# Optimization experiments

Measured on AMD Instinct MI355X. Metric: run time of the kernel, lower is better.

## Reference

```python
import jax, jax.numpy as jnp
import numpy as np

B, S, U, T = 64, 256, 1024, 512  # batch, max_sequence_size, units, output_token_length
W_SCALE = 0.02


def setup_inputs() -> dict:
    key = jax.random.key(0)
    ks = jax.random.split(key, 12)
    inp = {
        "h": jax.random.normal(ks[0], (B, S, U), jnp.float32),
        "s_0": jax.random.normal(ks[1], (B, U), jnp.float32),
        "Wy1": jax.random.normal(ks[2], (U, U), jnp.float32) * W_SCALE,
        "by1": jnp.zeros((U,), jnp.float32),
        "Wy2": jax.random.normal(ks[3], (U, T), jnp.float32) * W_SCALE,
        "by2": jnp.zeros((T,), jnp.float32),
        "We1": jax.random.normal(ks[4], (2 * U, U), jnp.float32) * W_SCALE,
        "be1": jnp.zeros((U,), jnp.float32),
        "We2": jax.random.normal(ks[5], (U, 1), jnp.float32) * W_SCALE,
        "be2": jnp.zeros((1,), jnp.float32),
        "Wf": jax.random.normal(ks[6], (T + U, U), jnp.float32) * W_SCALE,
        "bf": jnp.zeros((U,), jnp.float32),
        "Wi": jax.random.normal(ks[7], (T + U, U), jnp.float32) * W_SCALE,
        "bi": jnp.zeros((U,), jnp.float32),
        "Wg": jax.random.normal(ks[8], (T + U, U), jnp.float32) * W_SCALE,
        "bg": jnp.zeros((U,), jnp.float32),
        "Wo": jax.random.normal(ks[9], (T + U, U), jnp.float32) * W_SCALE,
        "bo": jnp.zeros((U,), jnp.float32),
    }
    return inp


def reference(h, s_0, Wy1, by1, Wy2, by2, We1, be1, We2, be2,
              Wf, bf, Wi, bi, Wg, bg, Wo, bo):
    # Precompute the h-dependent half of the first e_dense matmul once:
    # e_dense layer1 input is concat([h_i, s]) @ We1 = h_i @ We1[:U] + s @ We1[U:]
    We1_h, We1_s = We1[:U], We1[U:]
    h_proj = jnp.einsum('bsu,uv->bsv', h, We1_h)  # [B,S,U]

    def step(s, _):
        # y_dense: U -> U (tanh) -> T (linear)
        y = jnp.tanh(s @ Wy1 + by1) @ Wy2 + by2  # [B,T]
        # additive attention scores over all S encoder positions (vectorized)
        e1 = jax.nn.sigmoid(h_proj + (s @ We1_s + be1)[:, None, :])  # [B,S,U]
        e = jax.nn.sigmoid(jnp.squeeze(e1 @ We2, -1) + be2)          # [B,S]
        a = jax.nn.softmax(e, axis=-1)
        c = jnp.einsum('bsu,bs->bu', h, a)  # context vector [B,U]
        # LSTM cell with x = y, h = s, c = attention context
        x_h = jnp.concatenate([y, s], axis=-1)  # [B,T+U]
        i = jax.nn.sigmoid(x_h @ Wi + bi)
        f = jax.nn.sigmoid(x_h @ Wf + bf)
        o = jax.nn.sigmoid(x_h @ Wo + bo)
        g = jnp.tanh(x_h @ Wg + bg)
        c_new = f * c + i * g
        s_next = o * jnp.tanh(c_new)
        return s_next, y

    _, ys = jax.lax.scan(step, s_0, None, length=S)  # ys: [S,B,T]
    return jnp.transpose(ys, (1, 0, 2))  # [B,S,T]
```

## Files before the change

### kernel.cpp

```cpp
#include <hip/hip_runtime.h>
#include <hip/hip_bf16.h>

typedef __attribute__((ext_vector_type(4))) float floatx4;
typedef __attribute__((ext_vector_type(2))) float floatx2;
typedef __attribute__((ext_vector_type(8))) short shortx8;

#define NB 64
#define NS 256
#define NU 1024
#define NT 512

__device__ __forceinline__ unsigned short f2bf(float f){
  union{float f;unsigned u;}v; v.f=f;
  unsigned r = v.u + 0x7fffu + ((v.u>>16)&1u);
  return (unsigned short)(r>>16);
}
__device__ __forceinline__ float bf2f(unsigned short h){
  union{unsigned u;float f;}v; v.u = ((unsigned)h)<<16; return v.f;
}
__device__ __forceinline__ float sigf(float x){
  return __builtin_amdgcn_rcpf(1.f + __expf(-x));
}

__device__ __forceinline__ void cburst2x2f(floatx4 a[2], floatx4 b[2],
                                           const float* p0, const float* p1){
  asm volatile(
    "global_load_dwordx4 %0, %4, off sc0 sc1\n\t"
    "global_load_dwordx4 %1, %4, off offset:16 sc0 sc1\n\t"
    "global_load_dwordx4 %2, %5, off sc0 sc1\n\t"
    "global_load_dwordx4 %3, %5, off offset:16 sc0 sc1\n\t"
    "s_waitcnt vmcnt(0)"
    : "=&v"(a[0]),"=&v"(a[1]),"=&v"(b[0]),"=&v"(b[1])
    : "v"(p0),"v"(p1) : "memory");
}
__device__ __forceinline__ void cburst4d2(floatx2 o[4], const float* p0, const float* p1,
                                          const float* p2, const float* p3){
  asm volatile(
    "global_load_dwordx2 %0, %4, off sc0 sc1\n\t"
    "global_load_dwordx2 %1, %5, off sc0 sc1\n\t"
    "global_load_dwordx2 %2, %6, off sc0 sc1\n\t"
    "global_load_dwordx2 %3, %7, off sc0 sc1\n\t"
    "s_waitcnt vmcnt(0)"
    : "=&v"(o[0]),"=&v"(o[1]),"=&v"(o[2]),"=&v"(o[3])
    : "v"(p0),"v"(p1),"v"(p2),"v"(p3) : "memory");
}
__device__ __forceinline__ float cld_f32(const float* p){
  float v;
  asm volatile("global_load_dword %0, %1, off sc0 sc1\n\ts_waitcnt vmcnt(0)"
               : "=&v"(v) : "v"(p) : "memory");
  return v;
}
__device__ __forceinline__ void cst_u16(unsigned short* p, unsigned short v){
  asm volatile("global_store_short %0, %1, off sc0 sc1" :: "v"(p), "v"((unsigned)v) : "memory");
}
__device__ __forceinline__ void cst_f32(float* p, float v){
  asm volatile("global_store_dword %0, %1, off sc0 sc1" :: "v"(p), "v"(v) : "memory");
}
__device__ __forceinline__ void cst_u32(unsigned* p, unsigned v){
  asm volatile("global_store_dword %0, %1, off sc0 sc1" :: "v"(p), "v"(v) : "memory");
}

template<int MODE>
__global__ void gemm_sw(const unsigned short* __restrict__ A,
                        const unsigned short* __restrict__ Bsw,
                        void* __restrict__ Cout,
                        int M, int N, int K, int ldc,
                        const float* __restrict__ bias)
{
  const int lane = threadIdx.x & 63;
  const int lm = lane & 15, quad = lane >> 4;
  const int nwaves = (gridDim.x * blockDim.x) >> 6;
  const int w = (blockIdx.x * blockDim.x + threadIdx.x) >> 6;
  const int m64 = M >> 6, n64 = N >> 6, KS = K >> 5;
  const int ntask = m64 * n64;
  for (int task = w; task < ntask; task += nwaves) {
    const int mt = task % m64, nt = task / m64;
    floatx4 acc[4][4];
#pragma unroll
    for (int i=0;i<4;i++)
#pragma unroll
      for(int j=0;j<4;j++) acc[i][j] = (floatx4){0.f,0.f,0.f,0.f};
    const unsigned short* Ab = A + (size_t)(mt*64 + lm) * K + quad*8;
    for (int ks=0; ks<KS; ++ks) {
      shortx8 a[4], b[4];
#pragma unroll
      for (int i=0;i<4;i++)
        a[i] = *(const shortx8*)(Ab + (size_t)i*16*K + ks*32);
#pragma unroll
      for (int j=0;j<4;j++)
        b[j] = *(const shortx8*)(Bsw + (((size_t)(nt*4+j)*KS + ks)*64 + lane)*8);
#pragma unroll
      for (int i=0;i<4;i++)
#pragma unroll
        for (int j=0;j<4;j++)
          acc[i][j] = __builtin_amdgcn_mfma_f32_16x16x32_bf16(a[i], b[j], acc[i][j], 0,0,0);
    }
#pragma unroll
    for (int i=0;i<4;i++){
#pragma unroll
      for (int j=0;j<4;j++){
        const int col = nt*64 + j*16 + lm;
        const float bv = bias ? bias[col] : 0.f;
#pragma unroll
        for (int r=0;r<4;r++){
          const int row = mt*64 + i*16 + quad*4 + r;
          const float v = acc[i][j][r] + bv;
          if (MODE==0)      ((float*)Cout)[(size_t)row*ldc + col] = v;
          else if (MODE==1) ((unsigned short*)Cout)[(size_t)row*ldc + col] = f2bf(v);
          else { const int orow = (row&63)*NS + (row>>6);
                 ((float*)Cout)[(size_t)orow*ldc + col] = v; }
        }
      }
    }
  }
}

__global__ void conv_h(const float* __restrict__ src, unsigned short* __restrict__ dst, int n){
  for (int i = blockIdx.x*blockDim.x + threadIdx.x; i < n; i += gridDim.x*blockDim.x)
    dst[i] = f2bf(src[i]);
}

__global__ void conv_misc(const float* __restrict__ Wy2, const float* __restrict__ We2,
                          const float* __restrict__ s0, const float* __restrict__ by1,
                          const float* __restrict__ be1,
                          unsigned short* __restrict__ Wy2A, unsigned short* __restrict__ we2b,
                          unsigned short* __restrict__ s_bf, float* __restrict__ bz)
{
  int i = blockIdx.x*blockDim.x + threadIdx.x;
  if (i < 524288) Wy2A[i] = f2bf(Wy2[i]);
  else if (i < 525312) we2b[i-524288] = f2bf(We2[i-524288]);
  else if (i < 590848) s_bf[i-525312] = f2bf(s0[i-525312]);
  else if (i < 592896) { int n = i - 590848; bz[n] = (n<1024)? by1[n] : be1[n-1024]; }
}

__global__ void vbias_k(const float* __restrict__ by2,
                        const float* __restrict__ bi, const float* __restrict__ bff,
                        const float* __restrict__ bg, const float* __restrict__ bo,
                        const float* __restrict__ Wi, const float* __restrict__ Wf,
                        const float* __restrict__ Wg, const float* __restrict__ Wo,
                        float* __restrict__ vb)
{
  int i = blockIdx.x*blockDim.x + threadIdx.x;
  if (i >= 4096) return;
  int g = i >> 10, u = i & 1023;
  const float* bsrc = (g==0)?bi:(g==1)?bff:(g==2)?bg:bo;
  const float* W    = (g==0)?Wi:(g==1)?Wf:(g==2)?Wg:Wo;
  float s = bsrc[u];
  for (int tt = 0; tt < NT; ++tt) s += by2[tt] * W[(size_t)tt*NU + u];
  vb[i] = s;
}

__global__ void pack_b(const float* __restrict__ src, unsigned short* __restrict__ dst, int K, int N)
{
  const int KS = K >> 5;
  const size_t total = (size_t)K * N;
  for (size_t i = (size_t)blockIdx.x*blockDim.x + threadIdx.x; i < total;
       i += (size_t)gridDim.x*blockDim.x) {
    int j = i & 7; int lane = (i>>3) & 63; int r = (int)(i >> 9);
    int ks = r % KS; int nt = r / KS;
    int k = ks*32 + (lane>>4)*8 + j;
    int n = nt*16 + (lane&15);
    dst[i] = f2bf(src[(size_t)k*N + n]);
  }
}

__global__ void pack_a1(const float* __restrict__ Wy1, const float* __restrict__ We1,
                        unsigned short* __restrict__ dst)
{
  const int KS = 32;
  const size_t total = (size_t)1024*2048;
  for (size_t i = (size_t)blockIdx.x*blockDim.x + threadIdx.x; i < total;
       i += (size_t)gridDim.x*blockDim.x) {
    int j = i & 7; int lane = (i>>3) & 63; int r = (int)(i >> 9);
    int ks = r % KS; int nt = r / KS;
    int k = ks*32 + (lane>>4)*8 + j;
    int n = nt*16 + (lane&15);
    float v = (n < 1024) ? Wy1[(size_t)k*1024 + n]
                         : We1[(size_t)(1024+k)*1024 + (n-1024)];
    dst[i] = f2bf(v);
  }
}

__global__ void pack_wbig(const float* __restrict__ Mg,
                          const float* __restrict__ Wi, const float* __restrict__ Wf,
                          const float* __restrict__ Wg, const float* __restrict__ Wo,
                          unsigned short* __restrict__ dst)
{
  const int KS = 64;
  const size_t total = (size_t)2048*4096;
  for (size_t i = (size_t)blockIdx.x*blockDim.x + threadIdx.x; i < total;
       i += (size_t)gridDim.x*blockDim.x) {
    int j = i & 7; int lane = (i>>3) & 63; int r = (int)(i >> 9);
    int ks = r % KS; int nt = r / KS;
    int k = ks*32 + (lane>>4)*8 + j;
    int n = nt*16 + (lane&15);
    int g = n >> 10, u = n & 1023;
    float v;
    if (k < 1024) v = Mg[(size_t)g*1048576 + (size_t)k*1024 + u];
    else {
      const float* W = (g==0)?Wi:(g==1)?Wf:(g==2)?Wg:Wo;
      v = W[(size_t)(512 + k - 1024)*1024 + u];
    }
    dst[i] = f2bf(v);
  }
}

struct LoopArgs {
  unsigned short* s_all;
  unsigned short* tanh_all;
  const unsigned short* A1_sw;
  const unsigned short* Wbig_sw;
  const unsigned short* hproj;
  const float* h;
  const unsigned short* we2b;
  float* qbuf;
  float* watt;
  float* gates;
  const float* bz;
  const float* vbias;
  const float* be2;
  int* bar;
};

__global__ void __launch_bounds__(512, 2) loop_kernel(LoopArgs A)
{
  const int tid = threadIdx.x;
  const int bid = blockIdx.x;
  const int wid = tid >> 6;
  const int lane = tid & 63;
  const int lm = lane & 15, quad = lane >> 4;

  extern __shared__ floatx4 dynlds_v4[];
  unsigned char* const dynlds = (unsigned char*)dynlds_v4;

  int* gcnt = A.bar;
  int* root = A.bar + 16*32;
  int* genp = A.bar + 16*32 + 32;

  __shared__ float wsh[256];
  __shared__ float zparts[4];
  __shared__ float cbuf[512][2];

  auto gsync = [&]() {
    asm volatile("s_waitcnt vmcnt(0) lgkmcnt(0)" ::: "memory");
    __syncthreads();
    if (tid == 0) {
      int g = __hip_atomic_load(genp, __ATOMIC_RELAXED, __HIP_MEMORY_SCOPE_AGENT);
      int grp = bid >> 4;
      if (__hip_atomic_fetch_add(&gcnt[grp*32], 1, __ATOMIC_RELAXED, __HIP_MEMORY_SCOPE_AGENT) == 15) {
        __hip_atomic_store(&gcnt[grp*32], 0, __ATOMIC_RELAXED, __HIP_MEMORY_SCOPE_AGENT);
        if (__hip_atomic_fetch_add(root, 1, __ATOMIC_RELAXED, __HIP_MEMORY_SCOPE_AGENT) == 15) {
          __hip_atomic_store(root, 0, __ATOMIC_RELAXED, __HIP_MEMORY_SCOPE_AGENT);
          __hip_atomic_store(genp, g + 1, __ATOMIC_RELAXED, __HIP_MEMORY_SCOPE_AGENT);
        }
      }
      while (__hip_atomic_load(genp, __ATOMIC_RELAXED, __HIP_MEMORY_SCOPE_AGENT) == g)
        __builtin_amdgcn_s_sleep(1);
    }
    __syncthreads();
  };

  const int b3 = bid >> 2;
  const int j0_blk = (bid & 3) << 6;
  const int u3 = ((bid & 3) << 8) + (tid & 127) * 2;
  const int js3 = (tid >> 7) << 6;

  unsigned hreg[64];
  {
    const float* hb = A.h + (size_t)b3*NS*NU;
#pragma unroll
    for (int jj = 0; jj < 64; ++jj) {
      const floatx2 hv = *(const floatx2*)(hb + (size_t)(js3 + jj)*NU + u3);
      hreg[jj] = ((unsigned)f2bf(hv[0])) | (((unsigned)f2bf(hv[1])) << 16);
    }
  }
  {
    const unsigned char* hpg = (const unsigned char*)(A.hproj + ((size_t)(b3*NS + j0_blk))*NU);
#pragma unroll
    for (int it = 0; it < 16; ++it)
      *(floatx4*)(dynlds + it*8192 + tid*16) = *(const floatx4*)(hpg + it*8192 + tid*16);
  }
  float w2r[16];
  if (wid >= 4) {
    const shortx8 wa = *(const shortx8*)(A.we2b + 8*lane);
    const shortx8 wb = *(const shortx8*)(A.we2b + 512 + 8*lane);
#pragma unroll
    for (int i = 0; i < 8; ++i) {
      w2r[i]   = bf2f((unsigned short)wa[i]);
      w2r[8+i] = bf2f((unsigned short)wb[i]);
    }
  }
  const float be2v = A.be2[0];
  __syncthreads();

#pragma clang loop unroll(disable)
  for (int t = 0; t < NS; ++t) {
    const unsigned short* sbase = A.s_all + (size_t)t*(NB*NU);
    if (wid < 2) {
      const int task = bid*2 + wid;
      const int mt = task & 3, nt = task >> 2;
      floatx4 acc = (floatx4){0.f,0.f,0.f,0.f};
      const unsigned short* Ab = sbase + (mt*16 + lm)*NU + quad*8;
      for (int kb = 0; kb < 4; ++kb) {
        shortx8 a[8];
#pragma unroll
        for (int q = 0; q < 8; ++q) a[q] = *(const shortx8*)(Ab + kb*256 + q*32);
#pragma unroll
        for (int q = 0; q < 8; ++q) {
          shortx8 b = *(const shortx8*)(A.A1_sw + (((size_t)nt*32 + kb*8 + q)*64 + lane)*8);
          acc = __builtin_amdgcn_mfma_f32_16x16x32_bf16(a[q], b, acc, 0,0,0);
        }
      }
      const int col = nt*16 + lm;
      const float bzv = A.bz[col];
#pragma unroll
      for (int r = 0; r < 4; ++r) {
        const int row = mt*16 + quad*4 + r;
        const float v = acc[r] + bzv;
        if (col < NU) cst_u16(A.tanh_all + (size_t)t*(NB*NU) + row*NU + col, f2bf(tanhf(v)));
        else          cst_f32(A.qbuf + row*NU + (col - NU), v);
      }
    }
    gsync();
    if (wid < 4) {
      const int mt = wid, nt = bid;
      floatx4 acc = (floatx4){0.f,0.f,0.f,0.f};
      const int arow = mt*16 + lm;
      const unsigned short* tA = A.tanh_all + (size_t)t*(NB*NU) + arow*NU + quad*8;
      const unsigned short* sA = sbase + arow*NU + quad*8;
      for (int kb = 0; kb < 4; ++kb) {
        shortx8 a[8];
#pragma unroll
        for (int q = 0; q < 8; ++q) a[q] = *(const shortx8*)(tA + kb*256 + q*32);
#pragma unroll
        for (int q = 0; q < 8; ++q) {
          shortx8 b = *(const shortx8*)(A.Wbig_sw + (((size_t)nt*64 + kb*8 + q)*64 + lane)*8);
          acc = __builtin_amdgcn_mfma_f32_16x16x32_bf16(a[q], b, acc, 0,0,0);
        }
      }
      for (int kb = 0; kb < 4; ++kb) {
        shortx8 a[8];
#pragma unroll
        for (int q = 0; q < 8; ++q) a[q] = *(const shortx8*)(sA + kb*256 + q*32);
#pragma unroll
        for (int q = 0; q < 8; ++q) {
          shortx8 b = *(const shortx8*)(A.Wbig_sw + (((size_t)nt*64 + 32 + kb*8 + q)*64 + lane)*8);
          acc = __builtin_amdgcn_mfma_f32_16x16x32_bf16(a[q], b, acc, 0,0,0);
        }
      }
      const int col = nt*16 + lm;
      const float vb = A.vbias[col];
#pragma unroll
      for (int r = 0; r < 4; ++r) {
        const int row = mt*16 + quad*4 + r;
        cst_f32(A.gates + row*4096 + col, acc[r] + vb);
      }
    } else {
      const int aw = bid*4 + (wid - 4);
      const int b = aw >> 4;
      const int j0 = (aw & 15) << 4;
      floatx4 qa[2], qb[2];
      cburst2x2f(qa, qb, A.qbuf + b*NU + 8*lane, A.qbuf + b*NU + 512 + 8*lane);
      float qv[16];
#pragma unroll
      for (int i = 0; i < 4; ++i) {
        qv[i]    = qa[0][i]; qv[4+i]  = qa[1][i];
        qv[8+i]  = qb[0][i]; qv[12+i] = qb[1][i];
      }
      const int rbase = (wid - 4) * 16;
      for (int jj = 0; jj < 16; ++jj) {
        const int rl = rbase + jj;
        const shortx8 h0 = *(const shortx8*)(dynlds + rl*2048 + lane*16);
        const shortx8 h1 = *(const shortx8*)(dynlds + rl*2048 + 1024 + lane*16);
        float dot = 0.f;
#pragma unroll
        for (int i = 0; i < 8; ++i) {
          const float x = bf2f((unsigned short)h0[i]) + qv[i];
          dot += w2r[i] * sigf(x);
        }
#pragma unroll
        for (int i = 0; i < 8; ++i) {
          const float x = bf2f((unsigned short)h1[i]) + qv[8+i];
          dot += w2r[8+i] * sigf(x);
        }
#pragma unroll
        for (int off = 32; off > 0; off >>= 1) dot += __shfl_down(dot, off, 64);
        if (lane == 0) {
          const float e = 1.f/(1.f + __expf(-(dot + be2v)));
          cst_f32(A.watt + b*NS + (j0 + jj), __expf(e));
        }
      }
    }
    gsync();
    {
      const int b = bid >> 2, uc = (bid & 3) << 8;
      if (tid < 256) wsh[tid] = cld_f32(A.watt + b*NS + tid);
      __syncthreads();
      if (wid < 4) {
        float z = wsh[wid*64 + lane];
#pragma unroll
        for (int off = 32; off > 0; off >>= 1) z += __shfl_down(z, off, 64);
        if (lane == 0) zparts[wid] = z;
      }
      __syncthreads();
      const float invZ = __builtin_amdgcn_rcpf(zparts[0]+zparts[1]+zparts[2]+zparts[3]);
      float c0 = 0.f, c1 = 0.f;
#pragma unroll
      for (int jj = 0; jj < 64; ++jj) {
        const unsigned hv = hreg[jj];
        const float wv = wsh[js3 + jj];
        c0 += wv * bf2f((unsigned short)(hv & 0xffffu));
        c1 += wv * bf2f((unsigned short)(hv >> 16));
      }
      cbuf[tid][0] = c0; cbuf[tid][1] = c1;
      __syncthreads();
      if (tid < 128) {
        float cc0 = cbuf[tid][0] + cbuf[tid+128][0] + cbuf[tid+256][0] + cbuf[tid+384][0];
        float cc1 = cbuf[tid][1] + cbuf[tid+128][1] + cbuf[tid+256][1] + cbuf[tid+384][1];
        cc0 *= invZ; cc1 *= invZ;
        const int uu = uc + tid*2;
        const float* gp = A.gates + b*4096;
        floatx2 g4[4];
        cburst4d2(g4, gp + uu, gp + NU + uu, gp + 2*NU + uu, gp + 3*NU + uu);
        unsigned sout = 0;
#pragma unroll
        for (int p = 0; p < 2; ++p) {
          const float cx = p ? cc1 : cc0;
          const float iv = sigf(g4[0][p]);
          const float fv = sigf(g4[1][p]);
          const float gv = tanhf(g4[2][p]);
          const float ov = sigf(g4[3][p]);
          const float cn = fv*cx + iv*gv;
          const float sn = ov * tanhf(cn);
          sout |= ((unsigned)f2bf(sn)) << (16*p);
        }
        cst_u32((unsigned*)(A.s_all + (size_t)(t+1)*(NB*NU) + b*NU + uu), sout);
      }
    }
    gsync();
  }
}

extern "C" void kernel_launch(void* const* d_in, const int* in_sizes, int n_in,
                              void* d_out, int out_size, void* d_ws, size_t ws_size,
                              hipStream_t stream)
{
  const float* h   = (const float*)d_in[0];
  const float* s0  = (const float*)d_in[1];
  const float* Wy1 = (const float*)d_in[2];
  const float* by1 = (const float*)d_in[3];
  const float* Wy2 = (const float*)d_in[4];
  const float* by2 = (const float*)d_in[5];
  const float* We1 = (const float*)d_in[6];
  const float* be1 = (const float*)d_in[7];
  const float* We2 = (const float*)d_in[8];
  const float* be2 = (const float*)d_in[9];
  const float* Wf_p = (const float*)d_in[10];
  const float* bf_p = (const float*)d_in[11];
  const float* Wi_p = (const float*)d_in[12];
  const float* bi_p = (const float*)d_in[13];
  const float* Wg_p = (const float*)d_in[14];
  const float* bg_p = (const float*)d_in[15];
  const float* Wo_p = (const float*)d_in[16];
  const float* bo_p = (const float*)d_in[17];
  (void)in_sizes; (void)n_in; (void)out_size; (void)ws_size;

  char* ws = (char*)d_ws;
  size_t off = 0;
  auto alloc = [&](size_t bytes)->char*{
    char* p = ws + off; off = (off + bytes + 255) & ~(size_t)255; return p;
  };
  unsigned short* h_bf    = (unsigned short*)alloc((size_t)NB*NS*NU*2);
  unsigned short* hproj   = (unsigned short*)alloc((size_t)NB*NS*NU*2);
  unsigned short* tanh_all= (unsigned short*)alloc((size_t)NS*NB*NU*2);
  unsigned short* s_all   = (unsigned short*)alloc((size_t)(NS+1)*NB*NU*2);
  unsigned short* A1_sw   = (unsigned short*)alloc((size_t)NU*2048*2);
  unsigned short* Wbig_sw = (unsigned short*)alloc((size_t)2048*4096*2);
  unsigned short* We1h_sw = (unsigned short*)alloc((size_t)NU*NU*2);
  unsigned short* Wy2_sw  = (unsigned short*)alloc((size_t)NU*NT*2);
  unsigned short* we2b = (unsigned short*)alloc(NU*2);
  float* qbuf  = (float*)alloc((size_t)NB*NU*4);
  float* watt  = (float*)alloc((size_t)NB*NS*4);
  float* gates = (float*)alloc((size_t)NB*4096*4);
  float* bz    = (float*)alloc(2048*4);
  float* vbias = (float*)alloc(4096*4);
  int*   bar   = (int*)alloc(4096);
  float* Mg = (float*)tanh_all;
  unsigned short* Wy2A    = hproj;
  unsigned short* Wgtop_sw= hproj + (size_t)NU*NT;

  hipMemsetAsync(bar, 0, 4096, stream);

  conv_h<<<dim3(4096), dim3(256), 0, stream>>>(h, h_bf, NB*NS*NU);
  conv_misc<<<dim3(2316), dim3(256), 0, stream>>>(Wy2, We2, s0, by1, be1, Wy2A, we2b, s_all, bz);
  vbias_k<<<dim3(16), dim3(256), 0, stream>>>(by2, bi_p, bf_p, bg_p, bo_p,
                                              Wi_p, Wf_p, Wg_p, Wo_p, vbias);
  pack_b<<<dim3(1024), dim3(256), 0, stream>>>(We1, We1h_sw, 1024, 1024);
  pack_b<<<dim3(1024), dim3(256), 0, stream>>>(Wy2, Wy2_sw, 1024, 512);
  pack_b<<<dim3(512), dim3(256), 0, stream>>>(Wi_p, Wgtop_sw + 0*((size_t)NT*NU), 512, 1024);
  pack_b<<<dim3(512), dim3(256), 0, stream>>>(Wf_p, Wgtop_sw + 1*((size_t)NT*NU), 512, 1024);
  pack_b<<<dim3(512), dim3(256), 0, stream>>>(Wg_p, Wgtop_sw + 2*((size_t)NT*NU), 512, 1024);
  pack_b<<<dim3(512), dim3(256), 0, stream>>>(Wo_p, Wgtop_sw + 3*((size_t)NT*NU), 512, 1024);
  pack_a1<<<dim3(1024), dim3(256), 0, stream>>>(Wy1, We1, A1_sw);

  for (int g = 0; g < 4; ++g)
    gemm_sw<0><<<dim3(1024), dim3(256), 0, stream>>>(
        Wy2A, Wgtop_sw + (size_t)g*(NT*NU), Mg + (size_t)g*NU*NU,
        1024, 1024, 512, 1024, nullptr);
  pack_wbig<<<dim3(2048), dim3(256), 0, stream>>>(Mg, Wi_p, Wf_p, Wg_p, Wo_p, Wbig_sw);

  gemm_sw<1><<<dim3(1024), dim3(256), 0, stream>>>(
      h_bf, We1h_sw, hproj, NB*NS, 1024, 1024, 1024, nullptr);

  LoopArgs la;
  la.s_all = s_all; la.tanh_all = tanh_all; la.A1_sw = A1_sw; la.Wbig_sw = Wbig_sw;
  la.hproj = hproj; la.h = h; la.we2b = we2b;
  la.qbuf = qbuf; la.watt = watt; la.gates = gates;
  la.bz = bz; la.vbias = vbias; la.be2 = be2; la.bar = bar;
  loop_kernel<<<dim3(256), dim3(512), 131072, stream>>>(la);

  gemm_sw<2><<<dim3(1024), dim3(256), 0, stream>>>(
      tanh_all, Wy2_sw, d_out, NB*NS, 512, 1024, 512, by2);
}
```

Baseline: 15.24 ms.

## Double loop-kernel block size and split per-step GEMMs across more waves

Launches the persistent recurrent loop kernel with 1024 threads per block instead of 512. Per-step work is split across twice as many wavefronts: the first GEMM is split along K, the gate GEMM's tanh and state halves run on separate waves, and partial sums are combined through shared memory. The attention waves now read q from a shared-memory copy instead of issuing per-wave global bursts. The aim is to shorten the latency-bound serial critical path of each timestep. The cost is extra __syncthreads, fewer registers per thread, and the risk of lost occupancy or spills, since the hreg array is halved but the launch bound is now 1024.

```diff
diff --git a/kernel.cpp b/kernel.cpp
--- a/kernel.cpp
+++ b/kernel.cpp
@@ -22,16 +22,11 @@
   return __builtin_amdgcn_rcpf(1.f + __expf(-x));
 }
 
-__device__ __forceinline__ void cburst2x2f(floatx4 a[2], floatx4 b[2],
-                                           const float* p0, const float* p1){
-  asm volatile(
-    "global_load_dwordx4 %0, %4, off sc0 sc1\n\t"
-    "global_load_dwordx4 %1, %4, off offset:16 sc0 sc1\n\t"
-    "global_load_dwordx4 %2, %5, off sc0 sc1\n\t"
-    "global_load_dwordx4 %3, %5, off offset:16 sc0 sc1\n\t"
-    "s_waitcnt vmcnt(0)"
-    : "=&v"(a[0]),"=&v"(a[1]),"=&v"(b[0]),"=&v"(b[1])
-    : "v"(p0),"v"(p1) : "memory");
+__device__ __forceinline__ floatx4 cld_f32x4(const float* p){
+  floatx4 v;
+  asm volatile("global_load_dwordx4 %0, %1, off sc0 sc1\n\ts_waitcnt vmcnt(0)"
+               : "=&v"(v) : "v"(p) : "memory");
+  return v;
 }
 __device__ __forceinline__ void cburst4d2(floatx2 o[4], const float* p0, const float* p1,
                                           const float* p2, const float* p3){
@@ -222,7 +217,7 @@
   int* bar;
 };
 
-__global__ void __launch_bounds__(512, 2) loop_kernel(LoopArgs A)
+__global__ void __launch_bounds__(1024) loop_kernel(LoopArgs A)
 {
   const int tid = threadIdx.x;
   const int bid = blockIdx.x;
@@ -237,9 +232,11 @@
   int* root = A.bar + 16*32;
   int* genp = A.bar + 16*32 + 32;
 
+  __shared__ float qsh[1024];
+  __shared__ floatx4 pbuf[256];
   __shared__ float wsh[256];
   __shared__ float zparts[4];
-  __shared__ float cbuf[512][2];
+  __shared__ floatx2 cbuf[1024];
 
   auto gsync = [&]() {
     asm volatile("s_waitcnt vmcnt(0) lgkmcnt(0)" ::: "memory");
@@ -263,13 +260,13 @@
   const int b3 = bid >> 2;
   const int j0_blk = (bid & 3) << 6;
   const int u3 = ((bid & 3) << 8) + (tid & 127) * 2;
-  const int js3 = (tid >> 7) << 6;
-
-  unsigned hreg[64];
+  const int js3 = (tid >> 7) << 5;
+
+  unsigned hreg[32];
   {
     const float* hb = A.h + (size_t)b3*NS*NU;
 #pragma unroll
-    for (int jj = 0; jj < 64; ++jj) {
+    for (int jj = 0; jj < 32; ++jj) {
       const floatx2 hv = *(const floatx2*)(hb + (size_t)(js3 + jj)*NU + u3);
       hreg[jj] = ((unsigned)f2bf(hv[0])) | (((unsigned)f2bf(hv[1])) << 16);
     }
@@ -277,11 +274,11 @@
   {
     const unsigned char* hpg = (const unsigned char*)(A.hproj + ((size_t)(b3*NS + j0_blk))*NU);
 #pragma unroll
-    for (int it = 0; it < 16; ++it)
-      *(floatx4*)(dynlds + it*8192 + tid*16) = *(const floatx4*)(hpg + it*8192 + tid*16);
+    for (int it = 0; it < 8; ++it)
+      *(floatx4*)(dynlds + it*16384 + tid*16) = *(const floatx4*)(hpg + it*16384 + tid*16);
   }
   float w2r[16];
-  if (wid >= 4) {
+  if (wid >= 8) {
     const shortx8 wa = *(const shortx8*)(A.we2b + 8*lane);
     const shortx8 wb = *(const shortx8*)(A.we2b + 512 + 8*lane);
 #pragma unroll
@@ -296,104 +293,116 @@
 #pragma clang loop unroll(disable)
   for (int t = 0; t < NS; ++t) {
     const unsigned short* sbase = A.s_all + (size_t)t*(NB*NU);
-    if (wid < 2) {
-      const int task = bid*2 + wid;
-      const int mt = task & 3, nt = task >> 2;
-      floatx4 acc = (floatx4){0.f,0.f,0.f,0.f};
-      const unsigned short* Ab = sbase + (mt*16 + lm)*NU + quad*8;
-      for (int kb = 0; kb < 4; ++kb) {
-        shortx8 a[8];
-#pragma unroll
-        for (int q = 0; q < 8; ++q) a[q] = *(const shortx8*)(Ab + kb*256 + q*32);
-#pragma unroll
-        for (int q = 0; q < 8; ++q) {
-          shortx8 b = *(const shortx8*)(A.A1_sw + (((size_t)nt*32 + kb*8 + q)*64 + lane)*8);
-          acc = __builtin_amdgcn_mfma_f32_16x16x32_bf16(a[q], b, acc, 0,0,0);
-        }
-      }
-      const int col = nt*16 + lm;
-      const float bzv = A.bz[col];
-#pragma unroll
-      for (int r = 0; r < 4; ++r) {
-        const int row = mt*16 + quad*4 + r;
-        const float v = acc[r] + bzv;
-        if (col < NU) cst_u16(A.tanh_all + (size_t)t*(NB*NU) + row*NU + col, f2bf(tanhf(v)));
-        else          cst_f32(A.qbuf + row*NU + (col - NU), v);
-      }
-    }
-    gsync();
-    if (wid < 4) {
-      const int mt = wid, nt = bid;
-      floatx4 acc = (floatx4){0.f,0.f,0.f,0.f};
-      const int arow = mt*16 + lm;
-      const unsigned short* tA = A.tanh_all + (size_t)t*(NB*NU) + arow*NU + quad*8;
-      const unsigned short* sA = sbase + arow*NU + quad*8;
-      for (int kb = 0; kb < 4; ++kb) {
-        shortx8 a[8];
-#pragma unroll
-        for (int q = 0; q < 8; ++q) a[q] = *(const shortx8*)(tA + kb*256 + q*32);
-#pragma unroll
-        for (int q = 0; q < 8; ++q) {
-          shortx8 b = *(const shortx8*)(A.Wbig_sw + (((size_t)nt*64 + kb*8 + q)*64 + lane)*8);
-          acc = __builtin_amdgcn_mfma_f32_16x16x32_bf16(a[q], b, acc, 0,0,0);
-        }
-      }
-      for (int kb = 0; kb < 4; ++kb) {
-        shortx8 a[8];
-#pragma unroll
-        for (int q = 0; q < 8; ++q) a[q] = *(const shortx8*)(sA + kb*256 + q*32);
-#pragma unroll
-        for (int q = 0; q < 8; ++q) {
-          shortx8 b = *(const shortx8*)(A.Wbig_sw + (((size_t)nt*64 + 32 + kb*8 + q)*64 + lane)*8);
-          acc = __builtin_amdgcn_mfma_f32_16x16x32_bf16(a[q], b, acc, 0,0,0);
-        }
-      }
-      const int col = nt*16 + lm;
-      const float vb = A.vbias[col];
-#pragma unroll
-      for (int r = 0; r < 4; ++r) {
-        const int row = mt*16 + quad*4 + r;
-        cst_f32(A.gates + row*4096 + col, acc[r] + vb);
-      }
-    } else {
-      const int aw = bid*4 + (wid - 4);
-      const int b = aw >> 4;
-      const int j0 = (aw & 15) << 4;
-      floatx4 qa[2], qb[2];
-      cburst2x2f(qa, qb, A.qbuf + b*NU + 8*lane, A.qbuf + b*NU + 512 + 8*lane);
-      float qv[16];
-#pragma unroll
-      for (int i = 0; i < 4; ++i) {
-        qv[i]    = qa[0][i]; qv[4+i]  = qa[1][i];
-        qv[8+i]  = qb[0][i]; qv[12+i] = qb[1][i];
-      }
-      const int rbase = (wid - 4) * 16;
-      for (int jj = 0; jj < 16; ++jj) {
-        const int rl = rbase + jj;
-        const shortx8 h0 = *(const shortx8*)(dynlds + rl*2048 + lane*16);
-        const shortx8 h1 = *(const shortx8*)(dynlds + rl*2048 + 1024 + lane*16);
-        float dot = 0.f;
-#pragma unroll
-        for (int i = 0; i < 8; ++i) {
-          const float x = bf2f((unsigned short)h0[i]) + qv[i];
-          dot += w2r[i] * sigf(x);
-        }
-#pragma unroll
-        for (int i = 0; i < 8; ++i) {
-          const float x = bf2f((unsigned short)h1[i]) + qv[8+i];
-          dot += w2r[8+i] * sigf(x);
-        }
-#pragma unroll
-        for (int off = 32; off > 0; off >>= 1) dot += __shfl_down(dot, off, 64);
-        if (lane == 0) {
-          const float e = 1.f/(1.f + __expf(-(dot + be2v)));
-          cst_f32(A.watt + b*NS + (j0 + jj), __expf(e));
+    {
+      floatx4 accg = (floatx4){0.f,0.f,0.f,0.f};
+      if (wid < 4) {
+        const int task = bid*2 + (wid & 1);
+        const int mt = task & 3, nt = task >> 2;
+        const int kh = wid >> 1;
+        floatx4 acc = (floatx4){0.f,0.f,0.f,0.f};
+        const unsigned short* Ab = sbase + (mt*16 + lm)*NU + quad*8;
+        for (int k = 0; k < 2; ++k) {
+          const int kb = kh*2 + k;
+          shortx8 a[8];
+#pragma unroll
+          for (int q = 0; q < 8; ++q) a[q] = *(const shortx8*)(Ab + kb*256 + q*32);
+#pragma unroll
+          for (int q = 0; q < 8; ++q) {
+            shortx8 b = *(const shortx8*)(A.A1_sw + (((size_t)nt*32 + kb*8 + q)*64 + lane)*8);
+            acc = __builtin_amdgcn_mfma_f32_16x16x32_bf16(a[q], b, acc, 0,0,0);
+          }
+        }
+        if (wid >= 2) pbuf[(wid-2)*64 + lane] = acc; else accg = acc;
+      }
+      __syncthreads();
+      if (wid < 2) {
+        const int task = bid*2 + wid;
+        const int mt = task & 3, nt = task >> 2;
+        floatx4 acc = accg + pbuf[wid*64 + lane];
+        const int col = nt*16 + lm;
+        const float bzv = A.bz[col];
+#pragma unroll
+        for (int r = 0; r < 4; ++r) {
+          const int row = mt*16 + quad*4 + r;
+          const float v = acc[r] + bzv;
+          if (col < NU) cst_u16(A.tanh_all + (size_t)t*(NB*NU) + row*NU + col, f2bf(tanhf(v)));
+          else          cst_f32(A.qbuf + row*NU + (col - NU), v);
         }
       }
     }
     gsync();
     {
-      const int b = bid >> 2, uc = (bid & 3) << 8;
+      if (tid >= 512 && tid < 768) {
+        const int i = tid - 512;
+        *(floatx4*)&qsh[i*4] = cld_f32x4(A.qbuf + b3*NU + i*4);
+      }
+      __syncthreads();
+      floatx4 accg = (floatx4){0.f,0.f,0.f,0.f};
+      if (wid < 8) {
+        const int mt = wid & 3, nt = bid;
+        const int sel = wid >> 2;
+        floatx4 acc = (floatx4){0.f,0.f,0.f,0.f};
+        const int arow = mt*16 + lm;
+        const unsigned short* aA =
+            (sel ? sbase : A.tanh_all + (size_t)t*(NB*NU)) + arow*NU + quad*8;
+        const int bofs = sel ? 32 : 0;
+        for (int kb = 0; kb < 4; ++kb) {
+          shortx8 a[8];
+#pragma unroll
+          for (int q = 0; q < 8; ++q) a[q] = *(const shortx8*)(aA + kb*256 + q*32);
+#pragma unroll
+          for (int q = 0; q < 8; ++q) {
+            shortx8 b = *(const shortx8*)(A.Wbig_sw + (((size_t)nt*64 + bofs + kb*8 + q)*64 + lane)*8);
+            acc = __builtin_amdgcn_mfma_f32_16x16x32_bf16(a[q], b, acc, 0,0,0);
+          }
+        }
+        if (sel) pbuf[(wid-4)*64 + lane] = acc; else accg = acc;
+      } else {
+        const int rbase = (wid - 8) * 8;
+        float qv[16];
+#pragma unroll
+        for (int i = 0; i < 8; ++i) {
+          qv[i]   = qsh[8*lane + i];
+          qv[8+i] = qsh[512 + 8*lane + i];
+        }
+        for (int jj = 0; jj < 8; ++jj) {
+          const int rl = rbase + jj;
+          const shortx8 h0 = *(const shortx8*)(dynlds + rl*2048 + lane*16);
+          const shortx8 h1 = *(const shortx8*)(dynlds + rl*2048 + 1024 + lane*16);
+          float dot = 0.f;
+#pragma unroll
+          for (int i = 0; i < 8; ++i) {
+            const float x = bf2f((unsigned short)h0[i]) + qv[i];
+            dot += w2r[i] * sigf(x);
+          }
+#pragma unroll
+          for (int i = 0; i < 8; ++i) {
+            const float x = bf2f((unsigned short)h1[i]) + qv[8+i];
+            dot += w2r[8+i] * sigf(x);
+          }
+#pragma unroll
+          for (int off = 32; off > 0; off >>= 1) dot += __shfl_down(dot, off, 64);
+          if (lane == 0) {
+            const float e = 1.f/(1.f + __expf(-(dot + be2v)));
+            cst_f32(A.watt + b3*NS + (j0_blk + rl), __expf(e));
+          }
+        }
+      }
+      __syncthreads();
+      if (wid < 4) {
+        floatx4 acc = accg + pbuf[wid*64 + lane];
+        const int col = bid*16 + lm;
+        const float vb = A.vbias[col];
+#pragma unroll
+        for (int r = 0; r < 4; ++r) {
+          const int row = (wid&3)*16 + quad*4 + r;
+          cst_f32(A.gates + row*4096 + col, acc[r] + vb);
+        }
+      }
+    }
+    gsync();
+    {
+      const int b = b3, uc = (bid & 3) << 8;
       if (tid < 256) wsh[tid] = cld_f32(A.watt + b*NS + tid);
       __syncthreads();
       if (wid < 4) {
@@ -406,17 +415,21 @@
       const float invZ = __builtin_amdgcn_rcpf(zparts[0]+zparts[1]+zparts[2]+zparts[3]);
       float c0 = 0.f, c1 = 0.f;
 #pragma unroll
-      for (int jj = 0; jj < 64; ++jj) {
+      for (int jj = 0; jj < 32; ++jj) {
         const unsigned hv = hreg[jj];
         const float wv = wsh[js3 + jj];
         c0 += wv * bf2f((unsigned short)(hv & 0xffffu));
         c1 += wv * bf2f((unsigned short)(hv >> 16));
       }
-      cbuf[tid][0] = c0; cbuf[tid][1] = c1;
+      cbuf[tid] = (floatx2){c0, c1};
       __syncthreads();
       if (tid < 128) {
-        float cc0 = cbuf[tid][0] + cbuf[tid+128][0] + cbuf[tid+256][0] + cbuf[tid+384][0];
-        float cc1 = cbuf[tid][1] + cbuf[tid+128][1] + cbuf[tid+256][1] + cbuf[tid+384][1];
+        float cc0 = 0.f, cc1 = 0.f;
+#pragma unroll
+        for (int k = 0; k < 8; ++k) {
+          const floatx2 v = cbuf[tid + (k << 7)];
+          cc0 += v[0]; cc1 += v[1];
+        }
         cc0 *= invZ; cc1 *= invZ;
         const int uu = uc + tid*2;
         const float* gp = A.gates + b*4096;
@@ -517,7 +530,7 @@
   la.hproj = hproj; la.h = h; la.we2b = we2b;
   la.qbuf = qbuf; la.watt = watt; la.gates = gates;
   la.bz = bz; la.vbias = vbias; la.be2 = be2; la.bar = bar;
-  loop_kernel<<<dim3(256), dim3(512), 131072, stream>>>(la);
+  loop_kernel<<<dim3(256), dim3(1024), 131072, stream>>>(la);
 
   gemm_sw<2><<<dim3(1024), dim3(256), 0, stream>>>(
       tanh_all, Wy2_sw, d_out, NB*NS, 512, 1024, 512, by2);
```

New measurement: 12.27 ms (median of 2 runs). -19.5%, faster.
